# Optimization experiments

Hardware: AMD Instinct MI355X
Metric: run time of the kernel (lower is better)

## Reference

```python
import jax, jax.numpy as jnp
import numpy as np

N = 100000      # nodes
E = 1600000     # edges (before self-loops)
IN = 128        # in_channels
HID = 16        # hidden per head
HEADS = 8
OUT = 16        # out_channels (classes)
NEG_SLOPE = 0.2


def setup_inputs() -> dict:
    key = jax.random.key(0)
    ks = jax.random.split(key, 10)
    x = jax.random.normal(ks[0], (N, IN), jnp.float32)
    edge_index = jax.random.randint(ks[1], (2, E), 0, N, jnp.int32)
    g = lambda k, shape, fan: (jax.random.normal(k, shape, jnp.float32)
                               * (1.0 / np.sqrt(fan)).astype(np.float32))
    # layer 1: in -> heads*hid
    W1 = g(ks[2], (IN, HEADS * HID), IN)
    att_src1 = g(ks[3], (HEADS, HID), HID)
    att_dst1 = g(ks[4], (HEADS, HID), HID)
    b1 = jnp.zeros((HEADS * HID,), jnp.float32)
    # layer 2: heads*hid -> out, 1 head, concat=False
    W2 = g(ks[5], (HEADS * HID, OUT), HEADS * HID)
    att_src2 = g(ks[6], (1, OUT), OUT)
    att_dst2 = g(ks[7], (1, OUT), OUT)
    b2 = jnp.zeros((OUT,), jnp.float32)
    return dict(x=x, edge_index=edge_index, W1=W1, att_src1=att_src1,
                att_dst1=att_dst1, b1=b1, W2=W2, att_src2=att_src2,
                att_dst2=att_dst2, b2=b2)


def gat_conv(x, src, dst, W, a_src, a_dst, b, concat):
    """PyG-style GATConv (eval mode). src->dst message flow."""
    num_nodes = x.shape[0]
    H, C = a_src.shape
    h = (x @ W).reshape(num_nodes, H, C)                      # [N,H,C]
    # per-node attention halves, gathered to edges
    e = (h * a_src).sum(-1)[src] + (h * a_dst).sum(-1)[dst]   # [Etot,H]
    e = jax.nn.leaky_relu(e, NEG_SLOPE)
    # segment softmax over edges grouped by destination node
    emax = jax.ops.segment_max(e, dst, num_segments=num_nodes)    # [N,H]
    ee = jnp.exp(e - emax[dst])
    denom = jax.ops.segment_sum(ee, dst, num_segments=num_nodes)  # [N,H]
    alpha = ee / (denom[dst] + 1e-16)                              # [Etot,H]
    # weighted scatter-aggregate of source features
    msg = h[src] * alpha[:, :, None]                               # [Etot,H,C]
    out = jax.ops.segment_sum(msg, dst, num_segments=num_nodes)    # [N,H,C]
    out = out.reshape(num_nodes, H * C) if concat else out.mean(axis=1)
    return out + b


def reference(x, edge_index, W1, att_src1, att_dst1, b1,
              W2, att_src2, att_dst2, b2):
    # add self loops (PyG GATConv default)
    loop = jnp.arange(N, dtype=edge_index.dtype)
    src = jnp.concatenate([edge_index[0], loop])
    dst = jnp.concatenate([edge_index[1], loop])

    h = gat_conv(x, src, dst, W1, att_src1, att_dst1, b1, concat=True)
    embeddings = jax.nn.elu(h)
    logits = gat_conv(embeddings, src, dst, W2, att_src2, att_dst2, b2,
                      concat=False)
    return jax.nn.log_softmax(logits, axis=1), embeddings
```

## Files before the change

kernel.cpp:

```cpp
#include <hip/hip_runtime.h>
#include <hip/hip_bf16.h>
#include <math.h>

#define N_NODES 100000
#define E_EDGES 1600000
#define ETOT    (E_EDGES + N_NODES)
#define NEG     0.2f

#define SH        8
#define NBUCK     ((N_NODES + 255) >> 8)
#define BIN_TILE  4096
#define NBIN      ((E_EDGES + BIN_TILE - 1) / BIN_TILE)
#define CAP_B     5120

#define NMFMA     ((N_NODES + 63) / 64)

typedef __attribute__((ext_vector_type(8))) short bf16x8;
typedef __attribute__((ext_vector_type(4))) float f32x4;
typedef __attribute__((ext_vector_type(2))) short bf16p;

__device__ inline float lrelu(float x) { return x > 0.f ? x : NEG * x; }
__device__ inline float bflo(unsigned int b) { return __uint_as_float(b << 16); }
__device__ inline float bfhi(unsigned int b) { return __uint_as_float(b & 0xFFFF0000u); }
__device__ inline unsigned short f2bf(float f) {
    unsigned int u = __float_as_uint(f);
    return (unsigned short)((u + 0x7FFFu + ((u >> 16) & 1u)) >> 16);
}

__device__ inline float dot2bf(unsigned int wp, unsigned int hp, float c) {
#if __has_builtin(__builtin_amdgcn_fdot2_f32_bf16)
    return __builtin_amdgcn_fdot2_f32_bf16(__builtin_bit_cast(bf16p, wp),
                                           __builtin_bit_cast(bf16p, hp),
                                           c, false);
#else
    return fmaf(bflo(wp), bflo(hp), fmaf(bfhi(wp), bfhi(hp), c));
#endif
}

__global__ __launch_bounds__(256) void k_wt(const float* __restrict__ W,
                                            unsigned short* __restrict__ wtg) {
    int t = blockIdx.x * 256 + threadIdx.x;
    if (t >= 128 * 128) return;
    int n = t >> 7, k = t & 127;
    wtg[t] = f2bf(W[k * 128 + n]);
}

__global__ __launch_bounds__(256) void k_gemm1(
    const float* __restrict__ x, const unsigned short* __restrict__ wtg,
    const float* __restrict__ asrc, const float* __restrict__ adst,
    __hip_bfloat16* __restrict__ h1b, float* __restrict__ s1,
    float* __restrict__ d1) {
    __shared__ unsigned short xb[64][136];
    int t = threadIdx.x;
    int n0 = blockIdx.x * 64;

#pragma unroll
    for (int i = 0; i < 8; ++i) {
        int i4 = t + i * 256;
        int r = i4 >> 5;
        int c = (i4 & 31) * 4;
        float4 v = make_float4(0.f, 0.f, 0.f, 0.f);
        if (n0 + r < N_NODES) v = *(const float4*)(x + (size_t)(n0 + r) * 128 + c);
        xb[r][c + 0] = f2bf(v.x);
        xb[r][c + 1] = f2bf(v.y);
        xb[r][c + 2] = f2bf(v.z);
        xb[r][c + 3] = f2bf(v.w);
    }
    __syncthreads();

    int l = t & 63, wv = t >> 6;
    int col = l & 15, q4 = l >> 4;
    int rbase = wv * 16;
    int koff = q4 * 8;

    bf16x8 a[4];
#pragma unroll
    for (int st = 0; st < 4; ++st)
        a[st] = *(const bf16x8*)&xb[rbase + col][st * 32 + koff];

    int nodeb = n0 + rbase + q4 * 4;
#pragma unroll
    for (int nt = 0; nt < 8; ++nt) {
        f32x4 acc = {0.f, 0.f, 0.f, 0.f};
        const unsigned short* wrow = wtg + (size_t)(nt * 16 + col) * 128 + koff;
#pragma unroll
        for (int st = 0; st < 4; ++st) {
            bf16x8 b = *(const bf16x8*)(wrow + st * 32);
            acc = __builtin_amdgcn_mfma_f32_16x16x32_bf16(a[st], b, acc, 0, 0, 0);
        }
        float as_v = asrc[nt * 16 + col];
        float ad_v = adst[nt * 16 + col];
#pragma unroll
        for (int r = 0; r < 4; ++r) {
            int node = nodeb + r;
            if (node < N_NODES)
                h1b[(size_t)node * 128 + nt * 16 + col] = __float2bfloat16(acc[r]);
            float ps = acc[r] * as_v, pd = acc[r] * ad_v;
#pragma unroll
            for (int ofs = 1; ofs < 16; ofs <<= 1) {
                ps += __shfl_xor(ps, ofs, 64);
                pd += __shfl_xor(pd, ofs, 64);
            }
            if (col == 0 && node < N_NODES) {
                s1[node * 8 + nt] = ps;
                d1[node * 8 + nt] = pd;
            }
        }
    }
}

__global__ __launch_bounds__(256) void k_bin(
    const int* __restrict__ src, const int* __restrict__ dst,
    int* __restrict__ gcur, int2* __restrict__ coo) {
    __shared__ int2 st[BIN_TILE];
    __shared__ int  hist[NBUCK + 1];
    __shared__ int  lstart[NBUCK];
    __shared__ int  gbase[NBUCK];
    __shared__ int  tsum[256];
    int wb = blockIdx.x, t = threadIdx.x;
    int e0 = wb * BIN_TILE;
    int nE = min(BIN_TILE, E_EDGES - e0);
    for (int i = t; i <= NBUCK; i += 256) hist[i] = 0;
    __syncthreads();
    for (int i = t; i < nE; i += 256)
        atomicAdd(&hist[dst[e0 + i] >> SH], 1);
    __syncthreads();
    int i0 = 2 * t, i1 = 2 * t + 1;
    int h0 = (i0 < NBUCK) ? hist[i0] : 0;
    int h1v = (i1 < NBUCK) ? hist[i1] : 0;
    int s = h0 + h1v;
    tsum[t] = s;
    __syncthreads();
    for (int ofs = 1; ofs < 256; ofs <<= 1) {
        int u = (t >= ofs) ? tsum[t - ofs] : 0;
        __syncthreads();
        tsum[t] += u;
        __syncthreads();
    }
    int pre = tsum[t] - s;
    if (i0 < NBUCK) hist[i0] = pre;
    if (i1 < NBUCK) hist[i1] = pre + h0;
    if (t == 255) hist[NBUCK] = tsum[255];
    __syncthreads();
    for (int i = t; i < NBUCK; i += 256) {
        int st_ = hist[i];
        int cnt = hist[i + 1] - st_;
        lstart[i] = st_;
        if (cnt > 0) gbase[i] = i * CAP_B + atomicAdd(&gcur[i], cnt);
    }
    __syncthreads();
    for (int i = t; i < nE; i += 256) {
        int sv = src[e0 + i], dv = dst[e0 + i];
        int p = atomicAdd(&hist[dv >> SH], 1);
        st[p] = make_int2(sv, dv);
    }
    __syncthreads();
    for (int i = t; i < nE; i += 256) {
        int2 e = st[i];
        int b2 = e.y >> SH;
        int slot = gbase[b2] + (i - lstart[b2]);
        slot = min(slot, (b2 + 1) * CAP_B - 1);
        coo[slot] = e;
    }
}

__global__ __launch_bounds__(256) void k_scanb(const int* __restrict__ gcur,
                                               int* __restrict__ bbase,
                                               int* __restrict__ off) {
    __shared__ int tsum[256];
    int t = threadIdx.x;
    int i0 = 2 * t, i1 = 2 * t + 1;
    int a = 0, b = 0;
    if (i0 < NBUCK) a = min(gcur[i0], CAP_B) + min(256, N_NODES - (i0 << SH));
    if (i1 < NBUCK) b = min(gcur[i1], CAP_B) + min(256, N_NODES - (i1 << SH));
    int s = a + b;
    tsum[t] = s;
    __syncthreads();
    for (int ofs = 1; ofs < 256; ofs <<= 1) {
        int u = (t >= ofs) ? tsum[t - ofs] : 0;
        __syncthreads();
        tsum[t] += u;
        __syncthreads();
    }
    int pre = tsum[t] - s;
    if (i0 < NBUCK) bbase[i0] = pre;
    if (i1 < NBUCK) bbase[i1] = pre + a;
    if (t == 0) off[N_NODES] = ETOT;
}

__global__ __launch_bounds__(256) void k_fine(
    const int2* __restrict__ coo, const int* __restrict__ gcur,
    const int* __restrict__ bbase, int* __restrict__ off,
    int* __restrict__ csr) {
    __shared__ int ldeg[256];
    __shared__ int lpre[256];
    __shared__ int lsrc[CAP_B + 256];
    int b = blockIdx.x, t = threadIdx.x;
    int n0 = b << SH;
    int nn = min(256, N_NODES - n0);
    int ecnt = min(gcur[b], CAP_B);
    int base = bbase[b];
    const int2* seg = coo + (size_t)b * CAP_B;

    ldeg[t] = 0;
    __syncthreads();
    for (int i = t; i < ecnt; i += 256)
        atomicAdd(&ldeg[seg[i].y - n0], 1);
    __syncthreads();
    int d = (t < nn) ? ldeg[t] + 1 : 0;
    lpre[t] = d;
    __syncthreads();
    for (int ofs = 1; ofs < 256; ofs <<= 1) {
        int u = (t >= ofs) ? lpre[t - ofs] : 0;
        __syncthreads();
        lpre[t] += u;
        __syncthreads();
    }
    int myoff = lpre[t] - d;
    __syncthreads();
    if (t < nn) {
        off[n0 + t] = base + myoff;
        lsrc[myoff] = n0 + t;
        ldeg[t] = myoff + 1;
    }
    __syncthreads();
    for (int i = t; i < ecnt; i += 256) {
        int2 e = seg[i];
        int p = atomicAdd(&ldeg[e.y - n0], 1);
        lsrc[p] = e.x;
    }
    __syncthreads();
    int tot = ecnt + nn;
    for (int i = t; i < tot; i += 256)
        csr[base + i] = lsrc[i];
}

__global__ __launch_bounds__(256) void k_l1(
    const int* __restrict__ off, const int* __restrict__ csr,
    const float* __restrict__ s1, const float* __restrict__ d1,
    const uint4* __restrict__ h1q, const float* __restrict__ b1,
    float* __restrict__ emb) {
    int t = threadIdx.x;
    int node = blockIdx.x * 4 + (t >> 6);
    int l = t & 63;
    int g = l >> 4, q = l & 15;
    int hb = q >> 1;
    int lo = off[node], hi = off[node + 1];
    float dvh = d1[node * 8 + hb];

    float acc[8];
#pragma unroll
    for (int c = 0; c < 8; ++c) acc[c] = 0.f;
    float den = 0.f;

    int idx = lo + g;
    while (idx + 4 < hi) {
        int sa = csr[idx], sb = csr[idx + 4];
        uint4 ba = h1q[(size_t)sa * 16 + q];
        uint4 bb = h1q[(size_t)sb * 16 + q];
        float w0 = __expf(lrelu(s1[sa * 8 + hb] + dvh));
        float w1 = __expf(lrelu(s1[sb * 8 + hb] + dvh));
        den += w0 + w1;
        unsigned int wp;
        asm("v_cvt_pk_bf16_f32 %0, %1, %2" : "=v"(wp) : "v"(w0), "v"(w1));
        unsigned int p0, p1;
        p0 = __builtin_amdgcn_perm(bb.x, ba.x, 0x05040100u);
        p1 = __builtin_amdgcn_perm(bb.x, ba.x, 0x07060302u);
        acc[0] = dot2bf(wp, p0, acc[0]);
        acc[1] = dot2bf(wp, p1, acc[1]);
        p0 = __builtin_amdgcn_perm(bb.y, ba.y, 0x05040100u);
        p1 = __builtin_amdgcn_perm(bb.y, ba.y, 0x07060302u);
        acc[2] = dot2bf(wp, p0, acc[2]);
        acc[3] = dot2bf(wp, p1, acc[3]);
        p0 = __builtin_amdgcn_perm(bb.z, ba.z, 0x05040100u);
        p1 = __builtin_amdgcn_perm(bb.z, ba.z, 0x07060302u);
        acc[4] = dot2bf(wp, p0, acc[4]);
        acc[5] = dot2bf(wp, p1, acc[5]);
        p0 = __builtin_amdgcn_perm(bb.w, ba.w, 0x05040100u);
        p1 = __builtin_amdgcn_perm(bb.w, ba.w, 0x07060302u);
        acc[6] = dot2bf(wp, p0, acc[6]);
        acc[7] = dot2bf(wp, p1, acc[7]);
        idx += 8;
    }
    if (idx < hi) {
        int sc = csr[idx];
        uint4 bv = h1q[(size_t)sc * 16 + q];
        float w = __expf(lrelu(s1[sc * 8 + hb] + dvh));
        den += w;
        acc[0] = fmaf(w, bflo(bv.x), acc[0]);
        acc[1] = fmaf(w, bfhi(bv.x), acc[1]);
        acc[2] = fmaf(w, bflo(bv.y), acc[2]);
        acc[3] = fmaf(w, bfhi(bv.y), acc[3]);
        acc[4] = fmaf(w, bflo(bv.z), acc[4]);
        acc[5] = fmaf(w, bfhi(bv.z), acc[5]);
        acc[6] = fmaf(w, bflo(bv.w), acc[6]);
        acc[7] = fmaf(w, bfhi(bv.w), acc[7]);
    }
#pragma unroll
    for (int c = 0; c < 8; ++c) {
        acc[c] += __shfl_xor(acc[c], 16, 64);
        acc[c] += __shfl_xor(acc[c], 32, 64);
    }
    den += __shfl_xor(den, 16, 64);
    den += __shfl_xor(den, 32, 64);

    if (l < 16) {
        float r = 1.f / den;
        float vv[8];
#pragma unroll
        for (int c = 0; c < 8; ++c) {
            float v = acc[c] * r + b1[8 * q + c];
            vv[c] = v > 0.f ? v : expm1f(v);
        }
        float4* ep = (float4*)(emb + (size_t)node * 128);
        ep[2 * q]     = make_float4(vv[0], vv[1], vv[2], vv[3]);
        ep[2 * q + 1] = make_float4(vv[4], vv[5], vv[6], vv[7]);
    }
}

__global__ __launch_bounds__(256) void k_gemm2(
    const float* __restrict__ emb, const float* __restrict__ W,
    const float* __restrict__ asrc, const float* __restrict__ adst,
    __hip_bfloat16* __restrict__ h2b, float* __restrict__ s2,
    float* __restrict__ d2) {
    __shared__ float xs[16][129];
    int n0 = blockIdx.x * 16;
    int t = threadIdx.x;
#pragma unroll
    for (int i = 0; i < 8; ++i) {
        int idx = t + i * 256;
        xs[idx >> 7][idx & 127] = emb[(long)n0 * 128 + idx];
    }
    __syncthreads();
    int j = t & 15, sub = t >> 4;
    float acc = 0.f;
    for (int k = 0; k < 128; ++k) acc = fmaf(xs[sub][k], W[k * 16 + j], acc);
    int n = n0 + sub;
    h2b[(long)n * 16 + j] = __float2bfloat16(acc);
    float ps = acc * asrc[j], pd = acc * adst[j];
#pragma unroll
    for (int off = 8; off; off >>= 1) {
        ps += __shfl_down(ps, off, 16);
        pd += __shfl_down(pd, off, 16);
    }
    if (j == 0) { s2[n] = ps; d2[n] = pd; }
}

__global__ __launch_bounds__(256) void k_l2(
    const int* __restrict__ off, const int* __restrict__ csr,
    const float* __restrict__ s2, const float* __restrict__ d2,
    const unsigned int* __restrict__ h2w, const float* __restrict__ b2,
    float* __restrict__ logits) {
    int t = threadIdx.x;
    int node = blockIdx.x * 4 + (t >> 6);
    int l = t & 63;
    int g = l >> 3, p = l & 7;
    int lo = off[node], hi = off[node + 1];
    float dv = d2[node];

    float ax = 0.f, ay = 0.f, den = 0.f;
    for (int idx = lo + g; idx < hi; idx += 8) {
        int s = csr[idx];
        float w = __expf(lrelu(s2[s] + dv));
        den += w;
        unsigned int bv = h2w[(size_t)s * 8 + p];
        ax = fmaf(w, bflo(bv), ax);
        ay = fmaf(w, bfhi(bv), ay);
    }
#pragma unroll
    for (int ofs = 8; ofs < 64; ofs <<= 1) {
        ax += __shfl_xor(ax, ofs, 64);
        ay += __shfl_xor(ay, ofs, 64);
        den += __shfl_xor(den, ofs, 64);
    }
    float r = 1.f / den;
    float v0 = ax * r + b2[2 * p], v1 = ay * r + b2[2 * p + 1];
    float mm = fmaxf(v0, v1);
#pragma unroll
    for (int ofs = 1; ofs < 8; ofs <<= 1) mm = fmaxf(mm, __shfl_xor(mm, ofs, 8));
    float sm = __expf(v0 - mm) + __expf(v1 - mm);
#pragma unroll
    for (int ofs = 1; ofs < 8; ofs <<= 1) sm += __shfl_xor(sm, ofs, 8);
    if (g == 0) {
        float ls = logf(sm);
        logits[node * 16 + 2 * p]     = v0 - mm - ls;
        logits[node * 16 + 2 * p + 1] = v1 - mm - ls;
    }
}

extern "C" void kernel_launch(void* const* d_in, const int* in_sizes, int n_in,
                              void* d_out, int out_size, void* d_ws, size_t ws_size,
                              hipStream_t stream) {
    const float* x   = (const float*)d_in[0];
    const int*   ei  = (const int*)d_in[1];
    const float* W1  = (const float*)d_in[2];
    const float* as1 = (const float*)d_in[3];
    const float* ad1 = (const float*)d_in[4];
    const float* b1  = (const float*)d_in[5];
    const float* W2  = (const float*)d_in[6];
    const float* as2 = (const float*)d_in[7];
    const float* ad2 = (const float*)d_in[8];
    const float* b2  = (const float*)d_in[9];

    float* out    = (float*)d_out;
    float* logits = out;
    float* emb    = out + (size_t)N_NODES * 16;

    float* ws    = (float*)d_ws;
    unsigned int* h1w = (unsigned int*)ws;
    int2*  coo   = (int2*)(h1w + (size_t)N_NODES * 64);
    float* s1    = (float*)(coo + (size_t)NBUCK * CAP_B);
    float* d1    = s1 + (size_t)N_NODES * 8;
    unsigned int* h2w = (unsigned int*)(d1 + (size_t)N_NODES * 8);
    float* s2    = (float*)(h2w + (size_t)N_NODES * 8);
    float* d2v   = s2 + (size_t)N_NODES;
    int*   offs  = (int*)(d2v + (size_t)N_NODES);
    int*   csr   = offs + N_NODES + 2;
    int*   gcur  = csr + ETOT;
    int*   bbase = gcur + NBUCK;
    unsigned short* wtg = (unsigned short*)(bbase + NBUCK);

    const int* srcp = ei;
    const int* dstp = ei + E_EDGES;

    hipMemsetAsync(gcur, 0, (size_t)NBUCK * sizeof(int), stream);

    k_wt<<<64, 256, 0, stream>>>(W1, wtg);
    k_gemm1<<<NMFMA, 256, 0, stream>>>(x, wtg, as1, ad1,
                                       (__hip_bfloat16*)h1w, s1, d1);
    k_bin<<<NBIN, 256, 0, stream>>>(srcp, dstp, gcur, coo);
    k_scanb<<<1, 256, 0, stream>>>(gcur, bbase, offs);
    k_fine<<<NBUCK, 256, 0, stream>>>(coo, gcur, bbase, offs, csr);

    k_l1<<<N_NODES / 4, 256, 0, stream>>>(offs, csr, s1, d1,
                                          (const uint4*)h1w, b1, emb);

    k_gemm2<<<N_NODES / 16, 256, 0, stream>>>(emb, W2, as2, ad2,
                                              (__hip_bfloat16*)h2w, s2, d2v);
    k_l2<<<N_NODES / 4, 256, 0, stream>>>(offs, csr, s2, d2v, h2w, b2, logits);
}
```

Before: 266.2 us.

## Co-schedule GEMM1 tiles inside CSR build kernels and prefetch edges in layer 1

```diff
diff --git a/kernel.cpp b/kernel.cpp
--- a/kernel.cpp
+++ b/kernel.cpp
@@ -9,11 +9,13 @@
 
 #define SH        8
 #define NBUCK     ((N_NODES + 255) >> 8)
-#define BIN_TILE  4096
+#define BIN_TILE  2048
 #define NBIN      ((E_EDGES + BIN_TILE - 1) / BIN_TILE)
 #define CAP_B     5120
 
 #define NMFMA     ((N_NODES + 63) / 64)
+#define G_A       782
+#define G_B       (NMFMA - G_A)
 
 typedef __attribute__((ext_vector_type(8))) short bf16x8;
 typedef __attribute__((ext_vector_type(4))) float f32x4;
@@ -45,15 +47,12 @@
     wtg[t] = f2bf(W[k * 128 + n]);
 }
 
-__global__ __launch_bounds__(256) void k_gemm1(
+__device__ __forceinline__ void gemm1_role(
+    int n0, int t, unsigned short (*xb)[136],
     const float* __restrict__ x, const unsigned short* __restrict__ wtg,
     const float* __restrict__ asrc, const float* __restrict__ adst,
     __hip_bfloat16* __restrict__ h1b, float* __restrict__ s1,
     float* __restrict__ d1) {
-    __shared__ unsigned short xb[64][136];
-    int t = threadIdx.x;
-    int n0 = blockIdx.x * 64;
-
 #pragma unroll
     for (int i = 0; i < 8; ++i) {
         int i4 = t + i * 256;
@@ -109,56 +108,72 @@
     }
 }
 
-__global__ __launch_bounds__(256) void k_bin(
+union SmemBin {
+    struct {
+        int2 st[BIN_TILE];
+        int  hist[NBUCK + 1];
+        int  lstart[NBUCK];
+        int  gbase[NBUCK];
+        int  tsum[256];
+    } b;
+    unsigned short xb[64][136];
+};
+
+__global__ __launch_bounds__(256) void k_parBin(
     const int* __restrict__ src, const int* __restrict__ dst,
-    int* __restrict__ gcur, int2* __restrict__ coo) {
-    __shared__ int2 st[BIN_TILE];
-    __shared__ int  hist[NBUCK + 1];
-    __shared__ int  lstart[NBUCK];
-    __shared__ int  gbase[NBUCK];
-    __shared__ int  tsum[256];
-    int wb = blockIdx.x, t = threadIdx.x;
+    int* __restrict__ gcur, int2* __restrict__ coo,
+    const float* __restrict__ x, const unsigned short* __restrict__ wtg,
+    const float* __restrict__ asrc, const float* __restrict__ adst,
+    __hip_bfloat16* __restrict__ h1b, float* __restrict__ s1,
+    float* __restrict__ d1) {
+    __shared__ SmemBin sm;
+    int bid = blockIdx.x, t = threadIdx.x;
+    if (bid & 1) {
+        gemm1_role((bid >> 1) * 64, t, sm.xb, x, wtg, asrc, adst, h1b, s1, d1);
+        return;
+    }
+    int wb = bid >> 1;
     int e0 = wb * BIN_TILE;
     int nE = min(BIN_TILE, E_EDGES - e0);
-    for (int i = t; i <= NBUCK; i += 256) hist[i] = 0;
+    for (int i = t; i <= NBUCK; i += 256) sm.b.hist[i] = 0;
     __syncthreads();
     for (int i = t; i < nE; i += 256)
-        atomicAdd(&hist[dst[e0 + i] >> SH], 1);
+        atomicAdd(&sm.b.hist[dst[e0 + i] >> SH], 1);
     __syncthreads();
     int i0 = 2 * t, i1 = 2 * t + 1;
-    int h0 = (i0 < NBUCK) ? hist[i0] : 0;
-    int h1v = (i1 < NBUCK) ? hist[i1] : 0;
+    int h0 = (i0 < NBUCK) ? sm.b.hist[i0] : 0;
+    int h1v = (i1 < NBUCK) ? sm.b.hist[i1] : 0;
     int s = h0 + h1v;
-    tsum[t] = s;
+    sm.b.tsum[t] = s;
     __syncthreads();
     for (int ofs = 1; ofs < 256; ofs <<= 1) {
-        int u = (t >= ofs) ? tsum[t - ofs] : 0;
-        __syncthreads();
-        tsum[t] += u;
-        __syncthreads();
-    }
-    int pre = tsum[t] - s;
-    if (i0 < NBUCK) hist[i0] = pre;
-    if (i1 < NBUCK) hist[i1] = pre + h0;
-    if (t == 255) hist[NBUCK] = tsum[255];
+        int u = (t >= ofs) ? sm.b.tsum[t - ofs] : 0;
+        __syncthreads();
+        sm.b.tsum[t] += u;
+        __syncthreads();
+    }
+    int pre = sm.b.tsum[t] - s;
+    if (i0 < NBUCK) sm.b.hist[i0] = pre;
+    if (i1 < NBUCK) sm.b.hist[i1] = pre + h0;
+    if (t == 255) sm.b.hist[NBUCK] = sm.b.tsum[255];
     __syncthreads();
     for (int i = t; i < NBUCK; i += 256) {
-        int st_ = hist[i];
-        int cnt = hist[i + 1] - st_;
-        lstart[i] = st_;
-        if (cnt > 0) gbase[i] = i * CAP_B + atomicAdd(&gcur[i], cnt);
+        int st_ = sm.b.hist[i];
+        int cnt = sm.b.hist[i + 1] - st_;
+        sm.b.lstart[i] = st_;
+        if (cnt > 0) sm.b.gbase[i] = i * CAP_B + atomicAdd(&gcur[i], cnt);
     }
     __syncthreads();
     for (int i = t; i < nE; i += 256) {
         int sv = src[e0 + i], dv = dst[e0 + i];
-        int p = atomicAdd(&hist[dv >> SH], 1);
-        st[p] = make_int2(sv, dv);
+        int p = atomicAdd(&sm.b.hist[dv >> SH], 1);
+        sm.b.st[p] = make_int2(sv, dv);
     }
     __syncthreads();
     for (int i = t; i < nE; i += 256) {
-        int2 e = st[i];
+        int2 e = sm.b.st[i];
         int b2 = e.y >> SH;
-        int slot = gbase[b2] + (i - lstart[b2]);
+        int slot = sm.b.gbase[b2] + (i - sm.b.lstart[b2]);
         slot = min(slot, (b2 + 1) * CAP_B - 1);
         coo[slot] = e;
     }
@@ -188,51 +203,69 @@
     if (t == 0) off[N_NODES] = ETOT;
 }
 
-__global__ __launch_bounds__(256) void k_fine(
+union SmemFine {
+    struct {
+        int ldeg[256];
+        int lpre[256];
+        int lsrc[CAP_B + 256];
+    } f;
+    unsigned short xb[64][136];
+};
+
+__global__ __launch_bounds__(256) void k_parFine(
     const int2* __restrict__ coo, const int* __restrict__ gcur,
     const int* __restrict__ bbase, int* __restrict__ off,
-    int* __restrict__ csr) {
-    __shared__ int ldeg[256];
-    __shared__ int lpre[256];
-    __shared__ int lsrc[CAP_B + 256];
-    int b = blockIdx.x, t = threadIdx.x;
+    int* __restrict__ csr,
+    const float* __restrict__ x, const unsigned short* __restrict__ wtg,
+    const float* __restrict__ asrc, const float* __restrict__ adst,
+    __hip_bfloat16* __restrict__ h1b, float* __restrict__ s1,
+    float* __restrict__ d1) {
+    __shared__ SmemFine sm;
+    int bid = blockIdx.x, t = threadIdx.x;
+    bool isFine = (bid % 3 == 0) && (bid / 3 < NBUCK);
+    if (!isFine) {
+        int gid = bid - bid / 3 - 1;
+        gemm1_role((G_A + gid) * 64, t, sm.xb, x, wtg, asrc, adst, h1b, s1, d1);
+        return;
+    }
+    int b = bid / 3;
     int n0 = b << SH;
     int nn = min(256, N_NODES - n0);
     int ecnt = min(gcur[b], CAP_B);
     int base = bbase[b];
     const int2* seg = coo + (size_t)b * CAP_B;
 
-    ldeg[t] = 0;
+    sm.f.ldeg[t] = 0;
     __syncthreads();
     for (int i = t; i < ecnt; i += 256)
-        atomicAdd(&ldeg[seg[i].y - n0], 1);
-    __syncthreads();
-    int d = (t < nn) ? ldeg[t] + 1 : 0;
-    lpre[t] = d;
+        atomicAdd(&sm.f.ldeg[seg[i].y - n0], 1);
+    __syncthreads();
+    int d = (t < nn) ? sm.f.ldeg[t] + 1 : 0;
+    sm.f.lpre[t] = d;
     __syncthreads();
     for (int ofs = 1; ofs < 256; ofs <<= 1) {
-        int u = (t >= ofs) ? lpre[t - ofs] : 0;
-        __syncthreads();
-        lpre[t] += u;
-        __syncthreads();
-    }
-    int myoff = lpre[t] - d;
+        int u = (t >= ofs) ? sm.f.lpre[t - ofs] : 0;
+        __syncthreads();
+        sm.f.lpre[t] += u;
+        __syncthreads();
+    }
+    int myoff = sm.f.lpre[t] - d;
     __syncthreads();
     if (t < nn) {
         off[n0 + t] = base + myoff;
-        lsrc[myoff] = n0 + t;
-        ldeg[t] = myoff + 1;
+        sm.f.lsrc[myoff] = n0 + t;
+        sm.f.ldeg[t] = myoff + 1;
     }
     __syncthreads();
     for (int i = t; i < ecnt; i += 256) {
         int2 e = seg[i];
-        int p = atomicAdd(&ldeg[e.y - n0], 1);
-        lsrc[p] = e.x;
+        int p = atomicAdd(&sm.f.ldeg[e.y - n0], 1);
+        sm.f.lsrc[p] = e.x;
     }
     __syncthreads();
     int tot = ecnt + nn;
     for (int i = t; i < tot; i += 256)
-        csr[base + i] = lsrc[i];
+        csr[base + i] = sm.f.lsrc[i];
 }
 
 __global__ __launch_bounds__(256) void k_l1(
@@ -254,12 +287,32 @@
     float den = 0.f;
 
     int idx = lo + g;
-    while (idx + 4 < hi) {
-        int sa = csr[idx], sb = csr[idx + 4];
-        uint4 ba = h1q[(size_t)sa * 16 + q];
-        uint4 bb = h1q[(size_t)sb * 16 + q];
-        float w0 = __expf(lrelu(s1[sa * 8 + hb] + dvh));
-        float w1 = __expf(lrelu(s1[sb * 8 + hb] + dvh));
+    bool have = (idx + 4 < hi);
+    int sa = 0, sb = 0;
+    uint4 ba = make_uint4(0, 0, 0, 0), bb = make_uint4(0, 0, 0, 0);
+    float sva = 0.f, svb = 0.f;
+    if (have) {
+        sa = csr[idx]; sb = csr[idx + 4];
+        ba = h1q[(size_t)sa * 16 + q];
+        bb = h1q[(size_t)sb * 16 + q];
+        sva = s1[sa * 8 + hb];
+        svb = s1[sb * 8 + hb];
+    }
+    while (have) {
+        int nidx = idx + 8;
+        bool nhave = (nidx + 4 < hi);
+        int na = 0, nb = 0;
+        uint4 nba = make_uint4(0, 0, 0, 0), nbb = make_uint4(0, 0, 0, 0);
+        float nsa = 0.f, nsb = 0.f;
+        if (nhave) {
+            na = csr[nidx]; nb = csr[nidx + 4];
+            nba = h1q[(size_t)na * 16 + q];
+            nbb = h1q[(size_t)nb * 16 + q];
+            nsa = s1[na * 8 + hb];
+            nsb = s1[nb * 8 + hb];
+        }
+        float w0 = __expf(lrelu(sva + dvh));
+        float w1 = __expf(lrelu(svb + dvh));
         den += w0 + w1;
         unsigned int wp;
         asm("v_cvt_pk_bf16_f32 %0, %1, %2" : "=v"(wp) : "v"(w0), "v"(w1));
@@ -280,7 +333,8 @@
         p1 = __builtin_amdgcn_perm(bb.w, ba.w, 0x07060302u);
         acc[6] = dot2bf(wp, p0, acc[6]);
         acc[7] = dot2bf(wp, p1, acc[7]);
-        idx += 8;
+        sa = na; sb = nb; ba = nba; bb = nbb; sva = nsa; svb = nsb;
+        idx = nidx; have = nhave;
     }
     if (idx < hi) {
         int sc = csr[idx];
@@ -426,11 +480,13 @@
     hipMemsetAsync(gcur, 0, (size_t)NBUCK * sizeof(int), stream);
 
     k_wt<<<64, 256, 0, stream>>>(W1, wtg);
-    k_gemm1<<<NMFMA, 256, 0, stream>>>(x, wtg, as1, ad1,
-                                       (__hip_bfloat16*)h1w, s1, d1);
-    k_bin<<<NBIN, 256, 0, stream>>>(srcp, dstp, gcur, coo);
+    k_parBin<<<2 * NBIN, 256, 0, stream>>>(srcp, dstp, gcur, coo,
+                                           x, wtg, as1, ad1,
+                                           (__hip_bfloat16*)h1w, s1, d1);
     k_scanb<<<1, 256, 0, stream>>>(gcur, bbase, offs);
-    k_fine<<<NBUCK, 256, 0, stream>>>(coo, gcur, bbase, offs, csr);
+    k_parFine<<<NBUCK + G_B, 256, 0, stream>>>(coo, gcur, bbase, offs, csr,
+                                               x, wtg, as1, ad1,
+                                               (__hip_bfloat16*)h1w, s1, d1);
 
     k_l1<<<N_NODES / 4, 256, 0, stream>>>(offs, csr, s1, d1,
                                           (const uint4*)h1w, b1, emb);
```

Measured after the change: 259.3 us. 1.03x faster.
